# Kernel optimization log

Hardware: AMD Instinct MI355X
Metric: run time of the kernel (lower is better)

## Reference

```python
import jax, jax.numpy as jnp
import numpy as np

D_MODEL = 1024
C = 128
BATCH = 4
SEQ = 2048


def setup_inputs() -> dict:
    key = jax.random.key(0)
    k1, k2, k3, k4, k5 = jax.random.split(key, 5)
    x = jax.random.normal(k1, (BATCH, SEQ, D_MODEL), dtype=jnp.float32)
    # init_param_ uses fan-based scaling; emulate with scaled normals
    A = jax.random.normal(k2, (D_MODEL, C), dtype=jnp.float32) / np.sqrt(D_MODEL)
    Bmat = jax.random.normal(k3, (C, D_MODEL), dtype=jnp.float32) / np.sqrt(C)
    ov = jax.random.normal(k4, (D_MODEL, D_MODEL), dtype=jnp.float32) / np.sqrt(D_MODEL)
    mask = jax.random.uniform(k5, (BATCH, SEQ, C), dtype=jnp.float32)
    return {"x": x, "A": A, "Bmat": Bmat, "ov": ov, "mask": mask}


def reference(x, A, Bmat, ov, mask):
    # query_acts: [b, s, C], key_acts: [b, s, C]
    q = jnp.einsum('bsd,dc->bsc', x, A)
    k = jnp.einsum('bsd,cd->bsc', x, Bmat)
    # masked per-channel score reduction:
    # sum_c (q[b,q,c] * k[b,k,c] * mask[b,q,c]) == (q*mask) @ k^T
    scores = jnp.einsum('bqc,bkc->bqk', q * mask, k) / D_MODEL  # attn_scores_normed=True
    seq = x.shape[1]
    causal = jnp.triu(jnp.ones((seq, seq), dtype=bool), k=1)
    scores = jnp.where(causal[None, :, :], -jnp.inf, scores)
    patt = jax.nn.softmax(scores, axis=-1)  # [b, seqQ, seqK]
    z = jnp.einsum('bqk,bkd->bqd', patt, x)
    out = jnp.einsum('bqd,de->bqe', z, ov)
    return out
```

## Files before the change

kernel.cpp:

```cpp
#include <hip/hip_runtime.h>
#include <hip/hip_bf16.h>
#include <math.h>

#define D_MODEL 1024
#define C_DIM   128
#define BATCH   4
#define SEQ     2048
#define BS_ROWS (BATCH*SEQ)

typedef float  f32x4 __attribute__((ext_vector_type(4)));
typedef short  s16x8 __attribute__((ext_vector_type(8)));
typedef unsigned short u16;
typedef unsigned short u16x4 __attribute__((ext_vector_type(4)));

__device__ inline u16 f2bf(float f){
    unsigned u = __builtin_bit_cast(unsigned, f);
    u += 0x7FFF + ((u >> 16) & 1);
    return (u16)(u >> 16);
}

__device__ inline void gl_lds16(const u16* g, u16* l){
    __builtin_amdgcn_global_load_lds(
        (const __attribute__((address_space(1))) void*)g,
        (__attribute__((address_space(3))) void*)l,
        16, 0, 0);
}

template<int N> __device__ inline void wait_vm(){
    if constexpr (N <= 0)      asm volatile("s_waitcnt vmcnt(0)" ::: "memory");
    else if constexpr (N == 4) asm volatile("s_waitcnt vmcnt(4)" ::: "memory");
    else if constexpr (N == 8) asm volatile("s_waitcnt vmcnt(8)" ::: "memory");
    else                       asm volatile("s_waitcnt vmcnt(0)" ::: "memory");
}

template<int BM, int BN, int WM, int WN, int OUT_BF16, int MASK, int CSKIP,
         int CK, int QKF, int EXPSUM, int RSCALE, int ORD, int PAIR>
__launch_bounds__(WM*WN*64)
__global__ void gemm_bt(const u16* __restrict__ Ag, const u16* __restrict__ Bg,
                        const u16* __restrict__ Bg2,
                        void* __restrict__ Cg, void* __restrict__ Cg2,
                        const float* __restrict__ maskp,
                        float* __restrict__ rowsum,
                        int gx, int gy,
                        int K, int lda, int ldb, int ldc,
                        long sA, long sB, long sC, float scale)
{
    constexpr int W  = WM * WN;
    constexpr int PM = BM / WM, PN = BN / WN;
    constexpr int FM = PM / 16, FN = PN / 16;
    constexpr int CA = BM / 8 / W;
    constexpr int CB = BN / 8 / W;
    constexpr int NL = CA + CB;
    constexpr int ASZ = BM * 64, BSZ = BN * 64;
    __shared__ u16 As0[ASZ];
    __shared__ u16 As1[ASZ];
    __shared__ u16 Bs0[BSZ];
    __shared__ u16 Bs1[BSZ];

    const int nwg = gridDim.x;
    const int l   = (blockIdx.x & 7) * (nwg >> 3) + (blockIdx.x >> 3);
    int mt, nt, z, path = 0;
    if (PAIR == 1) {
        const int pairid = l & 7;
        const int f      = (l >> 5) & 1;
        mt = f ? (gx - 1 - pairid) : pairid;
        const int ntz = ((l >> 3) & 3) | (((l >> 6) & 7) << 2);
        nt = ntz & 7;
        z  = ntz >> 3;
    } else if (PAIR == 2) {
        const int f = (l >> 5) & 1;
        const int p = (l & 31) | ((l >> 6) << 5);
        z = p >> 7;
        const int q = p & 127;
        mt = f ? 15 - (q & 15) : (q & 15);
        nt = f ? 15 - (q >> 4) : (q >> 4);
    } else if (ORD == 0) {
        mt = l % gx; const int r = l / gx; nt = r % gy; z = r / gy;
    } else {
        nt = l % gy; const int r = l / gy; mt = r % gx; z = r / gx;
    }
    if (QKF) { constexpr int NT = C_DIM / BN; path = nt / NT; nt = nt % NT; }
    if (CSKIP && nt * BN >= (mt + 1) * BM) return;
    const u16* Aa = Ag + (long)z * sA;
    const u16* Bb = ((QKF && path) ? Bg2 : Bg) + (long)z * sB;
    const int tid = threadIdx.x, lane = tid & 63, wave = tid >> 6;
    const int wr = wave / WN, wc = wave % WN;
    const int mbase = mt * BM, nbase = nt * BN;
    int Keff = K;
    if (CK) { int ke = (mt + 1) * BM; Keff = ke < K ? ke : K; }
    const int nkt = Keff >> 6;

    f32x4 acc[FM][FN];
    #pragma unroll
    for (int m = 0; m < FM; ++m)
        #pragma unroll
        for (int n = 0; n < FN; ++n) acc[m][n] = (f32x4){0.f,0.f,0.f,0.f};

    const int sr  = lane >> 3;
    const int sc8 = (lane & 7) ^ sr;

    const u16* aptr[CA];
    const u16* bptr[CB];
    #pragma unroll
    for (int s = 0; s < CA; ++s)
        aptr[s] = Aa + (size_t)(mbase + (wave * CA + s) * 8 + sr) * lda + sc8 * 8;
    #pragma unroll
    for (int s = 0; s < CB; ++s)
        bptr[s] = Bb + (size_t)(nbase + (wave * CB + s) * 8 + sr) * ldb + sc8 * 8;

    auto STAGE = [&](u16 (&Ad)[ASZ], u16 (&Bd)[BSZ]) {
        #pragma unroll
        for (int s = 0; s < CA; ++s) { gl_lds16(aptr[s], &Ad[(wave * CA + s) * 512]); aptr[s] += 64; }
        #pragma unroll
        for (int s = 0; s < CB; ++s) { gl_lds16(bptr[s], &Bd[(wave * CB + s) * 512]); bptr[s] += 64; }
    };

    auto COMPUTE = [&](const u16 (&Ap)[ASZ], const u16 (&Bp)[BSZ]) {
        #pragma unroll
        for (int ks = 0; ks < 2; ++ks) {
            s16x8 af[FM], bfr[FN];
            const int k8 = ks * 4 + (lane >> 4);
            #pragma unroll
            for (int m = 0; m < FM; ++m) {
                const int row = wr * PM + m * 16 + (lane & 15);
                af[m] = *(const s16x8*)&Ap[row * 64 + ((k8 ^ (row & 7)) << 3)];
            }
            #pragma unroll
            for (int n = 0; n < FN; ++n) {
                const int row = wc * PN + n * 16 + (lane & 15);
                bfr[n] = *(const s16x8*)&Bp[row * 64 + ((k8 ^ (row & 7)) << 3)];
            }
            #pragma unroll
            for (int m = 0; m < FM; ++m)
                #pragma unroll
                for (int n = 0; n < FN; ++n)
                    acc[m][n] = __builtin_amdgcn_mfma_f32_16x16x32_bf16(af[m], bfr[n], acc[m][n], 0, 0, 0);
        }
    };

    STAGE(As0, Bs0);
    for (int t = 0; t < nkt; t += 2) {
        STAGE(As1, Bs1);
        wait_vm<NL>();
        __builtin_amdgcn_s_barrier();
        COMPUTE(As0, Bs0);
        __builtin_amdgcn_s_barrier();
        if (t + 2 < nkt) { STAGE(As0, Bs0); wait_vm<NL>(); }
        else             { wait_vm<0>(); }
        __builtin_amdgcn_s_barrier();
        COMPUTE(As1, Bs1);
        __builtin_amdgcn_s_barrier();
    }

    const bool kpath = QKF && path;
    void* Cout = kpath ? Cg2 : Cg;
    const int lr = (lane >> 4) * 4, lc = lane & 15;
    float rs[FM][4];
    if (EXPSUM) {
        #pragma unroll
        for (int m = 0; m < FM; ++m)
            #pragma unroll
            for (int r = 0; r < 4; ++r) rs[m][r] = 0.f;
    }
    #pragma unroll
    for (int m = 0; m < FM; ++m) {
        #pragma unroll
        for (int n = 0; n < FN; ++n) {
            const int gr = mbase + wr * PM + m * 16 + lr;
            const int gc = nbase + wc * PN + n * 16 + lc;
            #pragma unroll
            for (int r = 0; r < 4; ++r) {
                float f = acc[m][n][r] * scale;
                if (EXPSUM) {
                    f = (gc <= gr + r) ? __expf(f) : 0.f;
                    rs[m][r] += f;
                }
                if (RSCALE) f /= rowsum[(long)z * SEQ + gr + r];
                const size_t off = (size_t)(gr + r) * ldc + gc;
                if (MASK) { if (!kpath) f *= maskp[(long)z * sC + off]; }
                if (OUT_BF16) ((u16*)Cout + (long)z * sC)[off] = f2bf(f);
                else          ((float*)Cout + (long)z * sC)[off] = f;
            }
        }
    }
    if (EXPSUM) {
        #pragma unroll
        for (int m = 0; m < FM; ++m) {
            #pragma unroll
            for (int r = 0; r < 4; ++r) {
                float v = rs[m][r];
                v += __shfl_xor(v, 1); v += __shfl_xor(v, 2);
                v += __shfl_xor(v, 4); v += __shfl_xor(v, 8);
                if ((lane & 15) == 0) {
                    const int gr = mbase + wr * PM + m * 16 + lr + r;
                    atomicAdd(rowsum + (long)z * SEQ + gr, v);
                }
            }
        }
    }
}

__launch_bounds__(256)
__global__ void transpose_cvt(const float* __restrict__ in, u16* __restrict__ out,
                              int R, int Cc)
{
    __shared__ float t[32][33];
    const int c0 = blockIdx.x * 32, r0 = blockIdx.y * 32;
    const int tx = threadIdx.x & 31, ty = threadIdx.x >> 5;
    #pragma unroll
    for (int i = 0; i < 32; i += 8) t[ty + i][tx] = in[(size_t)(r0 + ty + i) * Cc + c0 + tx];
    __syncthreads();
    #pragma unroll
    for (int i = 0; i < 32; i += 8) out[(size_t)(c0 + ty + i) * R + r0 + tx] = f2bf(t[tx][ty + i]);
}

__launch_bounds__(256)
__global__ void convert_cvt(const float* __restrict__ in, u16* __restrict__ out,
                            int n4, float* __restrict__ rs, int rsn)
{
    const int gid = blockIdx.x * 256 + threadIdx.x;
    if (rs != nullptr && gid < rsn) rs[gid] = 0.f;
    for (int i = gid; i < n4; i += gridDim.x * 256) {
        float4 f = reinterpret_cast<const float4*>(in)[i];
        u16x4 o = { f2bf(f.x), f2bf(f.y), f2bf(f.z), f2bf(f.w) };
        reinterpret_cast<u16x4*>(out)[i] = o;
    }
}

extern "C" void kernel_launch(void* const* d_in, const int* in_sizes, int n_in,
                              void* d_out, int out_size, void* d_ws, size_t ws_size,
                              hipStream_t stream)
{
    const float* x    = (const float*)d_in[0];
    const float* A    = (const float*)d_in[1];
    const float* Bm   = (const float*)d_in[2];
    const float* ov   = (const float*)d_in[3];
    const float* mask = (const float*)d_in[4];

    char* w = (char*)d_ws;
    u16* xb   = (u16*)w; w += (size_t)BS_ROWS * D_MODEL * 2;
    u16* AbT  = (u16*)w; w += (size_t)C_DIM * D_MODEL * 2;
    u16* Bmb  = (u16*)w; w += (size_t)C_DIM * D_MODEL * 2;
    u16* ovT  = (u16*)w; w += (size_t)D_MODEL * D_MODEL * 2;
    u16* qm   = (u16*)w; w += (size_t)BS_ROWS * C_DIM * 2;
    u16* kk   = (u16*)w; w += (size_t)BS_ROWS * C_DIM * 2;
    u16* sc   = (u16*)w; w += (size_t)BATCH * SEQ * SEQ * 2;
    u16* xovT = (u16*)w; w += (size_t)D_MODEL * BS_ROWS * 2;
    float* rowsum = (float*)w; w += (size_t)BS_ROWS * 4;

    convert_cvt<<<2048, 256, 0, stream>>>(x, xb, BS_ROWS * D_MODEL / 4, rowsum, BS_ROWS);
    convert_cvt<<<128, 256, 0, stream>>>(Bm, Bmb, C_DIM * D_MODEL / 4, nullptr, 0);
    transpose_cvt<<<dim3(D_MODEL/32, D_MODEL/32, 1), 256, 0, stream>>>(ov, ovT, D_MODEL, D_MODEL);
    transpose_cvt<<<dim3(C_DIM/32, D_MODEL/32, 1), 256, 0, stream>>>(A, AbT, D_MODEL, C_DIM);

    gemm_bt<128,128,2,2, 1,0,0,0,0,0,0, 0,0><<<512, 256, 0, stream>>>(
        ovT, xb, nullptr, xovT, nullptr, nullptr, nullptr,
        8, 64,
        D_MODEL, D_MODEL, D_MODEL, BS_ROWS, 0, 0, 0, 1.0f);

    gemm_bt<64,64,2,2, 1,1,0,0,1,0,0, 1,0><<<512, 256, 0, stream>>>(
        xb, AbT, Bmb, qm, kk, mask, nullptr,
        128, 4,
        D_MODEL, D_MODEL, D_MODEL, C_DIM, 0, 0, 0, 1.0f);

    gemm_bt<128,128,2,2, 1,0,1,0,0,1,0, 1,2><<<1024, 256, 0, stream>>>(
        qm, kk, nullptr, sc, nullptr, nullptr, rowsum,
        16, 16,
        C_DIM, C_DIM, C_DIM, SEQ,
        (long)SEQ * C_DIM, (long)SEQ * C_DIM, (long)SEQ * SEQ, 1.0f / D_MODEL);

    gemm_bt<128,128,2,2, 0,0,0,1,0,0,1, 0,1><<<512, 256, 0, stream>>>(
        sc, xovT, nullptr, d_out, nullptr, nullptr, rowsum,
        16, 8,
        SEQ, SEQ, BS_ROWS, D_MODEL,
        (long)SEQ * SEQ, (long)SEQ , (long)SEQ * D_MODEL, 1.0f);
}
```

Before: 100.8 us.

## Merge causal scores GEMM and x·ov GEMM into one launch

The GEMM body is factored into a device function, and a new kernel runs the causal QK^T score tiles (blocks 0-1023) and the ov^T·x^T GEMM tiles (blocks 1024-1535) in a single grid. This removes one launch and lets the short, causally-skipped score tiles share the GPU with the large xov GEMM instead of running as separate serialized phases. The cost is a combined kernel whose register and LDS footprint is set by the worse of the two paths. The xov work also moves later in the stream, after the q/k projection.

```diff
diff --git a/kernel.cpp b/kernel.cpp
--- a/kernel.cpp
+++ b/kernel.cpp
@@ -33,17 +33,15 @@
     else                       asm volatile("s_waitcnt vmcnt(0)" ::: "memory");
 }
 
-template<int BM, int BN, int WM, int WN, int OUT_BF16, int MASK, int CSKIP,
-         int CK, int QKF, int EXPSUM, int RSCALE, int ORD, int PAIR>
-__launch_bounds__(WM*WN*64)
-__global__ void gemm_bt(const u16* __restrict__ Ag, const u16* __restrict__ Bg,
-                        const u16* __restrict__ Bg2,
-                        void* __restrict__ Cg, void* __restrict__ Cg2,
-                        const float* __restrict__ maskp,
-                        float* __restrict__ rowsum,
-                        int gx, int gy,
-                        int K, int lda, int ldb, int ldc,
-                        long sA, long sB, long sC, float scale)
+template<int BM, int BN, int WM, int WN, int OUT_BF16, int MASK, int CK,
+         int EXPSUM, int RSCALE>
+__device__ __forceinline__ void gemm_core(
+    u16 (&As0)[BM*64], u16 (&As1)[BM*64],
+    u16 (&Bs0)[BN*64], u16 (&Bs1)[BN*64],
+    const u16* __restrict__ Aa, const u16* __restrict__ Bb,
+    void* __restrict__ Cout, const float* __restrict__ mp,
+    float* __restrict__ rowsum,
+    int mt, int nt, int K, int lda, int ldb, int ldc, float scale)
 {
     constexpr int W  = WM * WN;
     constexpr int PM = BM / WM, PN = BN / WN;
@@ -52,37 +50,7 @@
     constexpr int CB = BN / 8 / W;
     constexpr int NL = CA + CB;
     constexpr int ASZ = BM * 64, BSZ = BN * 64;
-    __shared__ u16 As0[ASZ];
-    __shared__ u16 As1[ASZ];
-    __shared__ u16 Bs0[BSZ];
-    __shared__ u16 Bs1[BSZ];
-
-    const int nwg = gridDim.x;
-    const int l   = (blockIdx.x & 7) * (nwg >> 3) + (blockIdx.x >> 3);
-    int mt, nt, z, path = 0;
-    if (PAIR == 1) {
-        const int pairid = l & 7;
-        const int f      = (l >> 5) & 1;
-        mt = f ? (gx - 1 - pairid) : pairid;
-        const int ntz = ((l >> 3) & 3) | (((l >> 6) & 7) << 2);
-        nt = ntz & 7;
-        z  = ntz >> 3;
-    } else if (PAIR == 2) {
-        const int f = (l >> 5) & 1;
-        const int p = (l & 31) | ((l >> 6) << 5);
-        z = p >> 7;
-        const int q = p & 127;
-        mt = f ? 15 - (q & 15) : (q & 15);
-        nt = f ? 15 - (q >> 4) : (q >> 4);
-    } else if (ORD == 0) {
-        mt = l % gx; const int r = l / gx; nt = r % gy; z = r / gy;
-    } else {
-        nt = l % gy; const int r = l / gy; mt = r % gx; z = r / gx;
-    }
-    if (QKF) { constexpr int NT = C_DIM / BN; path = nt / NT; nt = nt % NT; }
-    if (CSKIP && nt * BN >= (mt + 1) * BM) return;
-    const u16* Aa = Ag + (long)z * sA;
-    const u16* Bb = ((QKF && path) ? Bg2 : Bg) + (long)z * sB;
+
     const int tid = threadIdx.x, lane = tid & 63, wave = tid >> 6;
     const int wr = wave / WN, wc = wave % WN;
     const int mbase = mt * BM, nbase = nt * BN;
@@ -152,8 +120,6 @@
         __builtin_amdgcn_s_barrier();
     }
 
-    const bool kpath = QKF && path;
-    void* Cout = kpath ? Cg2 : Cg;
     const int lr = (lane >> 4) * 4, lc = lane & 15;
     float rs[FM][4];
     if (EXPSUM) {
@@ -175,11 +141,11 @@
                     f = (gc <= gr + r) ? __expf(f) : 0.f;
                     rs[m][r] += f;
                 }
-                if (RSCALE) f /= rowsum[(long)z * SEQ + gr + r];
+                if (RSCALE) f /= rowsum[gr + r];
                 const size_t off = (size_t)(gr + r) * ldc + gc;
-                if (MASK) { if (!kpath) f *= maskp[(long)z * sC + off]; }
-                if (OUT_BF16) ((u16*)Cout + (long)z * sC)[off] = f2bf(f);
-                else          ((float*)Cout + (long)z * sC)[off] = f;
+                if (MASK) { if (mp) f *= mp[off]; }
+                if (OUT_BF16) ((u16*)Cout)[off] = f2bf(f);
+                else          ((float*)Cout)[off] = f;
             }
         }
     }
@@ -193,10 +159,104 @@
                 v += __shfl_xor(v, 4); v += __shfl_xor(v, 8);
                 if ((lane & 15) == 0) {
                     const int gr = mbase + wr * PM + m * 16 + lr + r;
-                    atomicAdd(rowsum + (long)z * SEQ + gr, v);
+                    atomicAdd(rowsum + gr, v);
                 }
             }
         }
+    }
+}
+
+template<int BM, int BN, int WM, int WN, int OUT_BF16, int MASK, int CSKIP,
+         int CK, int QKF, int EXPSUM, int RSCALE, int ORD, int PAIR>
+__launch_bounds__(WM*WN*64)
+__global__ void gemm_bt(const u16* __restrict__ Ag, const u16* __restrict__ Bg,
+                        const u16* __restrict__ Bg2,
+                        void* __restrict__ Cg, void* __restrict__ Cg2,
+                        const float* __restrict__ maskp,
+                        float* __restrict__ rowsum,
+                        int gx, int gy,
+                        int K, int lda, int ldb, int ldc,
+                        long sA, long sB, long sC, float scale)
+{
+    constexpr int ASZ = BM * 64, BSZ = BN * 64;
+    __shared__ u16 As0[ASZ];
+    __shared__ u16 As1[ASZ];
+    __shared__ u16 Bs0[BSZ];
+    __shared__ u16 Bs1[BSZ];
+
+    const int nwg = gridDim.x;
+    const int l   = (blockIdx.x & 7) * (nwg >> 3) + (blockIdx.x >> 3);
+    int mt, nt, z, path = 0;
+    if (PAIR == 1) {
+        const int pairid = l & 7;
+        const int f      = (l >> 5) & 1;
+        mt = f ? (gx - 1 - pairid) : pairid;
+        const int ntz = ((l >> 3) & 3) | (((l >> 6) & 7) << 2);
+        nt = ntz & 7;
+        z  = ntz >> 3;
+    } else if (ORD == 0) {
+        mt = l % gx; const int r = l / gx; nt = r % gy; z = r / gy;
+    } else {
+        nt = l % gy; const int r = l / gy; mt = r % gx; z = r / gx;
+    }
+    if (QKF) { constexpr int NT = C_DIM / BN; path = nt / NT; nt = nt % NT; }
+    if (CSKIP && nt * BN >= (mt + 1) * BM) return;
+
+    const bool kpath = QKF && path;
+    const u16* Aa = Ag + (long)z * sA;
+    const u16* Bb = (kpath ? Bg2 : Bg) + (long)z * sB;
+    void* CoutBase = kpath ? Cg2 : Cg;
+    void* Cout = OUT_BF16 ? (void*)((u16*)CoutBase + (long)z * sC)
+                          : (void*)((float*)CoutBase + (long)z * sC);
+    const float* mp = (MASK && !kpath && maskp) ? maskp + (long)z * sC : nullptr;
+    float* rsz = rowsum ? rowsum + (long)z * SEQ : nullptr;
+
+    gemm_core<BM,BN,WM,WN,OUT_BF16,MASK,CK,EXPSUM,RSCALE>(
+        As0, As1, Bs0, Bs1, Aa, Bb, Cout, mp, rsz,
+        mt, nt, K, lda, ldb, ldc, scale);
+}
+
+__launch_bounds__(256)
+__global__ void scores_xov_fused(const u16* __restrict__ qm,
+                                 const u16* __restrict__ kk,
+                                 u16* __restrict__ sc,
+                                 float* __restrict__ rowsum,
+                                 const u16* __restrict__ ovT,
+                                 const u16* __restrict__ xb,
+                                 u16* __restrict__ xovT)
+{
+    __shared__ u16 As0[128*64];
+    __shared__ u16 As1[128*64];
+    __shared__ u16 Bs0[128*64];
+    __shared__ u16 Bs1[128*64];
+
+    const int bid = blockIdx.x;
+    if (bid < 1024) {
+        const int l = (bid & 7) * 128 + (bid >> 3);
+        const int f = (l >> 5) & 1;
+        const int p = (l & 31) | ((l >> 6) << 5);
+        const int z = p >> 7;
+        const int q = p & 127;
+        const int mt = f ? 15 - (q & 15) : (q & 15);
+        const int nt = f ? 15 - (q >> 4) : (q >> 4);
+        if (nt > mt) return;
+        gemm_core<128,128,2,2, 1,0,0,1,0>(
+            As0, As1, Bs0, Bs1,
+            qm + (long)z * SEQ * C_DIM,
+            kk + (long)z * SEQ * C_DIM,
+            sc + (long)z * SEQ * SEQ,
+            nullptr,
+            rowsum + (long)z * SEQ,
+            mt, nt, C_DIM, C_DIM, C_DIM, SEQ, 1.0f / D_MODEL);
+    } else {
+        const int local = bid - 1024;
+        const int l = (local & 7) * 64 + (local >> 3);
+        const int mt = l % 8;
+        const int nt = l / 8;
+        gemm_core<128,128,2,2, 1,0,0,0,0>(
+            As0, As1, Bs0, Bs1,
+            ovT, xb, xovT, nullptr, nullptr,
+            mt, nt, D_MODEL, D_MODEL, D_MODEL, BS_ROWS, 1.0f);
     }
 }
 
@@ -253,21 +313,12 @@
     transpose_cvt<<<dim3(D_MODEL/32, D_MODEL/32, 1), 256, 0, stream>>>(ov, ovT, D_MODEL, D_MODEL);
     transpose_cvt<<<dim3(C_DIM/32, D_MODEL/32, 1), 256, 0, stream>>>(A, AbT, D_MODEL, C_DIM);
 
-    gemm_bt<128,128,2,2, 1,0,0,0,0,0,0, 0,0><<<512, 256, 0, stream>>>(
-        ovT, xb, nullptr, xovT, nullptr, nullptr, nullptr,
-        8, 64,
-        D_MODEL, D_MODEL, D_MODEL, BS_ROWS, 0, 0, 0, 1.0f);
-
     gemm_bt<64,64,2,2, 1,1,0,0,1,0,0, 1,0><<<512, 256, 0, stream>>>(
         xb, AbT, Bmb, qm, kk, mask, nullptr,
         128, 4,
         D_MODEL, D_MODEL, D_MODEL, C_DIM, 0, 0, 0, 1.0f);
 
-    gemm_bt<128,128,2,2, 1,0,1,0,0,1,0, 1,2><<<1024, 256, 0, stream>>>(
-        qm, kk, nullptr, sc, nullptr, nullptr, rowsum,
-        16, 16,
-        C_DIM, C_DIM, C_DIM, SEQ,
-        (long)SEQ * C_DIM, (long)SEQ * C_DIM, (long)SEQ * SEQ, 1.0f / D_MODEL);
+    scores_xov_fused<<<1536, 256, 0, stream>>>(qm, kk, sc, rowsum, ovT, xb, xovT);
 
     gemm_bt<128,128,2,2, 0,0,0,1,0,0,1, 0,1><<<512, 256, 0, stream>>>(
         sc, xovT, nullptr, d_out, nullptr, nullptr, rowsum,
```

Result: faster. 94.37 us (-6.4%).
